# Optimization experiments

Hardware: AMD Instinct MI355X
Metric: run time of the kernel (lower is better)

Reference implementation:

```python
import jax, jax.numpy as jnp
import numpy as np

ALPHA = 0.2          # LeakyReLU negative slope
NEG_INF = -9e15      # mask value used by the torch module


def setup_inputs() -> dict:
    key = jax.random.key(0)
    k1, k2, k3, k4 = jax.random.split(key, 4)
    N, F_IN, F_OUT = 8192, 128, 128
    h = jax.random.normal(k1, (N, F_IN), dtype=jnp.float32)
    adj = jax.random.randint(k2, (N, N), 0, 2, dtype=jnp.int32)
    # xavier_uniform(gain=1.414) approximated with scaled normal init
    W = jax.random.normal(k3, (F_IN, F_OUT), dtype=jnp.float32) * (1.414 / np.sqrt(F_IN))
    a = jax.random.normal(k4, (2 * F_OUT, 1), dtype=jnp.float32) * (1.414 / np.sqrt(2 * F_OUT))
    return {"h": h, "adj": adj, "W": W, "a": a}


def reference(h, adj, W, a):
    # Wh: [N, F]
    Wh = h @ W
    F_out = W.shape[1]
    # e[i,j] = LeakyReLU( [Wh_i || Wh_j] . a ) = LeakyReLU( Wh_i.a1 + Wh_j.a2 )
    e_src = Wh @ a[:F_out, 0]   # [N]
    e_dst = Wh @ a[F_out:, 0]   # [N]
    e = jax.nn.leaky_relu(e_src[:, None] + e_dst[None, :], negative_slope=ALPHA)  # [N, N]
    attention = jax.nn.softmax(jnp.where(adj > 0, e, NEG_INF), axis=1)
    # dropout is identity in eval mode
    h_prime = attention @ Wh    # [N, F]
    return h_prime
```

## Files before the change

kernel.cpp:

```cpp
#include <hip/hip_runtime.h>
#include <hip/hip_bf16.h>


#define NN 8192
#define FF 128
#define SEG 4
#define JSEG (NN / SEG)
#define ITERS (JSEG / 64)

typedef __bf16 bf16x8 __attribute__((ext_vector_type(8)));
typedef float floatx4 __attribute__((ext_vector_type(4)));
typedef int   intx4  __attribute__((ext_vector_type(4)));

__device__ __forceinline__ unsigned short b2u(__bf16 x) {
    return __builtin_bit_cast(unsigned short, x);
}

__global__ __launch_bounds__(512) void k1_wh(const float* __restrict__ h,
                                             const float* __restrict__ W,
                                             const float* __restrict__ a,
                                             unsigned short* __restrict__ WhT,
                                             float* __restrict__ e_src,
                                             float* __restrict__ e_dst) {
    __shared__ float hL[32 * 132];
    __shared__ float wL[128 * 132];
    __shared__ float uL[128], vL[128];
    __shared__ unsigned short tL[128 * 40];

    int t = threadIdx.x;
    int i0 = blockIdx.x * 32;

    {
        int row = t >> 4, c = (t & 15) * 8;
        const float4* s = (const float4*)&h[(i0 + row) * FF + c];
        float4* d = (float4*)&hL[row * 132 + c];
        d[0] = s[0]; d[1] = s[1];
    }
    {
        int row = t >> 2, c = (t & 3) * 32;
        const float4* s = (const float4*)&W[row * FF + c];
        float4* d = (float4*)&wL[row * 132 + c];
        #pragma unroll
        for (int j = 0; j < 8; j++) d[j] = s[j];
    }
    __syncthreads();

    if (t < 256) {
        int k = t & 127;
        const float* ap = a + (t >> 7) * FF;
        float s = 0.f;
        for (int c = 0; c < 128; c += 4) {
            float4 w4 = *(const float4*)&wL[k * 132 + c];
            s = fmaf(w4.x, ap[c], s);     s = fmaf(w4.y, ap[c + 1], s);
            s = fmaf(w4.z, ap[c + 2], s); s = fmaf(w4.w, ap[c + 3], s);
        }
        (t < 128 ? uL : vL)[k] = s * 1.44269504f;
    }

    int r0 = (t & 7) * 4;
    int c0 = (t >> 3) * 2;
    float acc[4][2] = {};
    for (int k0 = 0; k0 < 128; k0 += 4) {
        float4 hr[4]; float2 wr[4];
        #pragma unroll
        for (int i = 0; i < 4; i++) hr[i] = *(const float4*)&hL[(r0 + i) * 132 + k0];
        #pragma unroll
        for (int i = 0; i < 4; i++) wr[i] = *(const float2*)&wL[(k0 + i) * 132 + c0];
        #pragma unroll
        for (int kj = 0; kj < 4; kj++) {
            #pragma unroll
            for (int ri = 0; ri < 4; ri++) {
                float hvv = ((const float*)&hr[ri])[kj];
                acc[ri][0] = fmaf(hvv, wr[kj].x, acc[ri][0]);
                acc[ri][1] = fmaf(hvv, wr[kj].y, acc[ri][1]);
            }
        }
    }
    #pragma unroll
    for (int ri = 0; ri < 4; ri++)
        #pragma unroll
        for (int cj = 0; cj < 2; cj++)
            tL[(c0 + cj) * 40 + r0 + ri] = b2u((__bf16)acc[ri][cj]);
    __syncthreads();

    if (t < 64) {
        int row = t & 31;
        const float* sv = (t < 32) ? uL : vL;
        float s = 0.f;
        for (int k = 0; k < 128; k += 4) {
            float4 h4 = *(const float4*)&hL[row * 132 + k];
            float4 s4 = *(const float4*)&sv[k];
            s = fmaf(h4.x, s4.x, s); s = fmaf(h4.y, s4.y, s);
            s = fmaf(h4.z, s4.z, s); s = fmaf(h4.w, s4.w, s);
        }
        (t < 32 ? e_src : e_dst)[i0 + row] = s;
    }
    {
        int f = t & 127, part = t >> 7;
        const uint4* s = (const uint4*)&tL[f * 40 + part * 8];
        uint4* d = (uint4*)&WhT[f * NN + i0 + part * 8];
        *d = *s;
    }
}

__device__ __forceinline__ float mask_w(int a, float x) {
    float l = fmaxf(x, 0.2f * x);
    float e = __builtin_amdgcn_exp2f(l);
    return a > 0 ? e : 0.f;
}

__device__ __forceinline__ ushort4 pack4(float w0, float w1, float w2, float w3) {
    union { ushort4 u; __bf16 b[4]; } pk;
    pk.b[0] = (__bf16)w0; pk.b[1] = (__bf16)w1;
    pk.b[2] = (__bf16)w2; pk.b[3] = (__bf16)w3;
    return pk.u;
}

__global__ __launch_bounds__(512, 4) void k2_gat(const int* __restrict__ adj,
                                                 const unsigned short* __restrict__ WhT,
                                                 const float* __restrict__ e_src,
                                                 const float* __restrict__ e_dst,
                                                 float* __restrict__ numpart,
                                                 float* __restrict__ denpart) {
    __shared__ unsigned short wt[2][32 * 64];
    __shared__ float esL[32];
    __shared__ float dpart[32 * 17];

    int t = threadIdx.x;
    int bx = blockIdx.x;
    int g = bx >> 2, seg = bx & 3;
    int i0 = g * 32;
    int jbase = seg * JSEG;

    if (t < 32) esL[t] = e_src[i0 + t];

    int q  = t & 15;
    int ii = t >> 4;
    int lane = t & 63, wave = t >> 6;
    int mrow = lane & 15, quad = lane >> 4;
    int n0 = wave * 16;

    const unsigned short* Bb = WhT + (size_t)(n0 + mrow) * NN + jbase + quad * 8;
    const intx4* Ab = (const intx4*)(adj + (size_t)(i0 + ii) * NN + jbase + q * 4);
    const float* Eb = e_dst + jbase + q * 4;

    int waddr = ii * 64 + (((q >> 1) ^ (ii & 7)) << 3) + ((q & 1) << 2);
    int ra00 = mrow * 64 + ((quad ^ (mrow & 7)) << 3);
    int ra01 = mrow * 64 + (((4 + quad) ^ (mrow & 7)) << 3);
    int ra10 = (16 + mrow) * 64 + ((quad ^ (mrow & 7)) << 3);
    int ra11 = (16 + mrow) * 64 + (((4 + quad) ^ (mrow & 7)) << 3);

    floatx4 acc0 = {0.f, 0.f, 0.f, 0.f};
    floatx4 acc1 = {0.f, 0.f, 0.f, 0.f};
    float dsum = 0.f;

    intx4  av0 = __builtin_nontemporal_load(Ab);
    float4 ed0 = *(const float4*)Eb;
    intx4  avB = __builtin_nontemporal_load(Ab + 16);
    float4 edB = *(const float4*)(Eb + 64);
    bf16x8 b0 = *(const bf16x8*)Bb;
    bf16x8 b1 = *(const bf16x8*)(Bb + 32);

    __syncthreads();
    float es_i = esL[ii];

    {
        float w0 = mask_w(av0.x, es_i + ed0.x);
        float w1 = mask_w(av0.y, es_i + ed0.y);
        float w2 = mask_w(av0.z, es_i + ed0.z);
        float w3 = mask_w(av0.w, es_i + ed0.w);
        dsum += (w0 + w1) + (w2 + w3);
        *(ushort4*)&wt[0][waddr] = pack4(w0, w1, w2, w3);
    }
    __syncthreads();

    for (int k = 0; k < ITERS - 1; k++) {
        int jp = ((k + 2 < ITERS) ? (k + 2) : (ITERS - 1));
        intx4  avN = __builtin_nontemporal_load(Ab + jp * 16);
        float4 edN = *(const float4*)(Eb + jp * 64);
        int jn = (k + 1) * 64;
        bf16x8 nb0 = *(const bf16x8*)(Bb + jn);
        bf16x8 nb1 = *(const bf16x8*)(Bb + jn + 32);

        const unsigned short* buf = wt[k & 1];
        bf16x8 a00 = *(const bf16x8*)&buf[ra00];
        bf16x8 a10 = *(const bf16x8*)&buf[ra10];
        bf16x8 a01 = *(const bf16x8*)&buf[ra01];
        bf16x8 a11 = *(const bf16x8*)&buf[ra11];
        acc0 = __builtin_amdgcn_mfma_f32_16x16x32_bf16(a00, b0, acc0, 0, 0, 0);
        acc1 = __builtin_amdgcn_mfma_f32_16x16x32_bf16(a10, b0, acc1, 0, 0, 0);
        acc0 = __builtin_amdgcn_mfma_f32_16x16x32_bf16(a01, b1, acc0, 0, 0, 0);
        acc1 = __builtin_amdgcn_mfma_f32_16x16x32_bf16(a11, b1, acc1, 0, 0, 0);

        float w0 = mask_w(avB.x, es_i + edB.x);
        float w1 = mask_w(avB.y, es_i + edB.y);
        float w2 = mask_w(avB.z, es_i + edB.z);
        float w3 = mask_w(avB.w, es_i + edB.w);
        dsum += (w0 + w1) + (w2 + w3);
        *(ushort4*)&wt[(k + 1) & 1][waddr] = pack4(w0, w1, w2, w3);
        avB = avN; edB = edN;
        b0 = nb0; b1 = nb1;
        __syncthreads();
    }
    {
        const unsigned short* buf = wt[(ITERS - 1) & 1];
        bf16x8 a00 = *(const bf16x8*)&buf[ra00];
        bf16x8 a10 = *(const bf16x8*)&buf[ra10];
        bf16x8 a01 = *(const bf16x8*)&buf[ra01];
        bf16x8 a11 = *(const bf16x8*)&buf[ra11];
        acc0 = __builtin_amdgcn_mfma_f32_16x16x32_bf16(a00, b0, acc0, 0, 0, 0);
        acc1 = __builtin_amdgcn_mfma_f32_16x16x32_bf16(a10, b0, acc1, 0, 0, 0);
        acc0 = __builtin_amdgcn_mfma_f32_16x16x32_bf16(a01, b1, acc0, 0, 0, 0);
        acc1 = __builtin_amdgcn_mfma_f32_16x16x32_bf16(a11, b1, acc1, 0, 0, 0);
    }

    dpart[ii * 17 + q] = dsum;
    __syncthreads();
    if (t < 32) {
        float s = 0.f;
        #pragma unroll
        for (int k = 0; k < 16; k++) s += dpart[t * 17 + k];
        __builtin_nontemporal_store(s, &denpart[seg * NN + i0 + t]);
    }

    float* np = numpart + (size_t)seg * NN * FF;
    #pragma unroll
    for (int r = 0; r < 4; r++) {
        int row0 = quad * 4 + r;
        __builtin_nontemporal_store(acc0[r], &np[(size_t)(i0 + row0) * FF + n0 + mrow]);
        __builtin_nontemporal_store(acc1[r], &np[(size_t)(i0 + 16 + row0) * FF + n0 + mrow]);
    }
}

__global__ __launch_bounds__(256) void k3_merge(const float* __restrict__ np,
                                               const float* __restrict__ dp,
                                               float* __restrict__ out) {
    int idx = blockIdx.x * 256 + threadIdx.x;
    int i = idx >> 5;
    int c = (idx & 31) << 2;
    float d = dp[i] + dp[NN + i] + dp[2 * NN + i] + dp[3 * NN + i];
    float r = 1.0f / d;
    size_t o = (size_t)i * FF + c;
    const size_t S = (size_t)NN * FF;
    float4 a0 = *(const float4*)&np[o];
    float4 a1 = *(const float4*)&np[o + S];
    float4 a2 = *(const float4*)&np[o + 2 * S];
    float4 a3 = *(const float4*)&np[o + 3 * S];
    float4 v;
    v.x = ((a0.x + a1.x) + (a2.x + a3.x)) * r;
    v.y = ((a0.y + a1.y) + (a2.y + a3.y)) * r;
    v.z = ((a0.z + a1.z) + (a2.z + a3.z)) * r;
    v.w = ((a0.w + a1.w) + (a2.w + a3.w)) * r;
    *(float4*)&out[o] = v;
}

extern "C" void kernel_launch(void* const* d_in, const int* in_sizes, int n_in,
                              void* d_out, int out_size, void* d_ws, size_t ws_size,
                              hipStream_t stream) {
    const float* h   = (const float*)d_in[0];
    const int*   adj = (const int*)d_in[1];
    const float* W   = (const float*)d_in[2];
    const float* a   = (const float*)d_in[3];
    float* out = (float*)d_out;

    char* ws = (char*)d_ws;
    unsigned short* WhT = (unsigned short*)ws;
    float* e_src = (float*)(ws + 2097152);
    float* e_dst = e_src + NN;
    float* denpart = e_dst + NN;
    float* numpart = (float*)(ws + (4u << 20));

    k1_wh<<<dim3(256), dim3(512), 0, stream>>>(h, W, a, WhT, e_src, e_dst);
    k2_gat<<<dim3(256 * SEG), dim3(512), 0, stream>>>(adj, WhT, e_src, e_dst, numpart, denpart);
    k3_merge<<<dim3(NN * FF / 4 / 256), dim3(256), 0, stream>>>(numpart, denpart, out);
}
```

Before: 397.8 us.

## Drop split-K segments and fuse normalization into the attention kernel

Removes the 4-way split over the neighbour dimension and the separate merge kernel. Each block now handles 16 rows across the full 8192 columns with 128-wide tiles and writes normalized output directly, with the denominator reduced by wave shuffles. This avoids the numerator and denominator partial buffers and their round trip through global memory. In exchange, each block now owns only 16 rows, so the WhT B-operand is re-read from global memory by twice as many row blocks. The B loads are also no longer prefetched one iteration ahead.

```diff
diff --git a/kernel.cpp b/kernel.cpp
--- a/kernel.cpp
+++ b/kernel.cpp
@@ -4,9 +4,7 @@
 
 #define NN 8192
 #define FF 128
-#define SEG 4
-#define JSEG (NN / SEG)
-#define ITERS (JSEG / 64)
+#define ITERS (NN / 128)
 
 typedef __bf16 bf16x8 __attribute__((ext_vector_type(8)));
 typedef float floatx4 __attribute__((ext_vector_type(4)));
@@ -120,46 +118,39 @@
                                                  const unsigned short* __restrict__ WhT,
                                                  const float* __restrict__ e_src,
                                                  const float* __restrict__ e_dst,
-                                                 float* __restrict__ numpart,
-                                                 float* __restrict__ denpart) {
-    __shared__ unsigned short wt[2][32 * 64];
-    __shared__ float esL[32];
-    __shared__ float dpart[32 * 17];
+                                                 float* __restrict__ out) {
+    __shared__ unsigned short wt[2][16 * 128];
+    __shared__ float esL[16];
+    __shared__ float denL[16];
 
     int t = threadIdx.x;
-    int bx = blockIdx.x;
-    int g = bx >> 2, seg = bx & 3;
-    int i0 = g * 32;
-    int jbase = seg * JSEG;
-
-    if (t < 32) esL[t] = e_src[i0 + t];
-
-    int q  = t & 15;
-    int ii = t >> 4;
+    int i0 = blockIdx.x * 16;
+
+    if (t < 16) esL[t] = e_src[i0 + t];
+
+    int q  = t & 31;
+    int ii = t >> 5;
     int lane = t & 63, wave = t >> 6;
     int mrow = lane & 15, quad = lane >> 4;
     int n0 = wave * 16;
 
-    const unsigned short* Bb = WhT + (size_t)(n0 + mrow) * NN + jbase + quad * 8;
-    const intx4* Ab = (const intx4*)(adj + (size_t)(i0 + ii) * NN + jbase + q * 4);
-    const float* Eb = e_dst + jbase + q * 4;
-
-    int waddr = ii * 64 + (((q >> 1) ^ (ii & 7)) << 3) + ((q & 1) << 2);
-    int ra00 = mrow * 64 + ((quad ^ (mrow & 7)) << 3);
-    int ra01 = mrow * 64 + (((4 + quad) ^ (mrow & 7)) << 3);
-    int ra10 = (16 + mrow) * 64 + ((quad ^ (mrow & 7)) << 3);
-    int ra11 = (16 + mrow) * 64 + (((4 + quad) ^ (mrow & 7)) << 3);
-
-    floatx4 acc0 = {0.f, 0.f, 0.f, 0.f};
-    floatx4 acc1 = {0.f, 0.f, 0.f, 0.f};
+    const unsigned short* Bb = WhT + (size_t)(n0 + mrow) * NN + quad * 8;
+    const intx4* Ab = (const intx4*)(adj + (size_t)(i0 + ii) * NN + q * 4);
+    const float* Eb = e_dst + q * 4;
+
+    int waddr = ii * 128 + (((q >> 1) ^ (ii & 7)) << 3) + ((q & 1) << 2);
+    int ra0 = mrow * 128 + (((0 + quad) ^ (mrow & 7)) << 3);
+    int ra1 = mrow * 128 + (((4 + quad) ^ (mrow & 7)) << 3);
+    int ra2 = mrow * 128 + (((8 + quad) ^ (mrow & 7)) << 3);
+    int ra3 = mrow * 128 + (((12 + quad) ^ (mrow & 7)) << 3);
+
+    floatx4 acc = {0.f, 0.f, 0.f, 0.f};
     float dsum = 0.f;
 
     intx4  av0 = __builtin_nontemporal_load(Ab);
     float4 ed0 = *(const float4*)Eb;
-    intx4  avB = __builtin_nontemporal_load(Ab + 16);
-    float4 edB = *(const float4*)(Eb + 64);
-    bf16x8 b0 = *(const bf16x8*)Bb;
-    bf16x8 b1 = *(const bf16x8*)(Bb + 32);
+    intx4  avB = __builtin_nontemporal_load(Ab + 32);
+    float4 edB = *(const float4*)(Eb + 128);
 
     __syncthreads();
     float es_i = esL[ii];
@@ -176,21 +167,24 @@
 
     for (int k = 0; k < ITERS - 1; k++) {
         int jp = ((k + 2 < ITERS) ? (k + 2) : (ITERS - 1));
-        intx4  avN = __builtin_nontemporal_load(Ab + jp * 16);
-        float4 edN = *(const float4*)(Eb + jp * 64);
-        int jn = (k + 1) * 64;
-        bf16x8 nb0 = *(const bf16x8*)(Bb + jn);
-        bf16x8 nb1 = *(const bf16x8*)(Bb + jn + 32);
+        intx4  avN = __builtin_nontemporal_load(Ab + jp * 32);
+        float4 edN = *(const float4*)(Eb + jp * 128);
+
+        int j0 = k * 128;
+        bf16x8 b0 = *(const bf16x8*)(Bb + j0);
+        bf16x8 b1 = *(const bf16x8*)(Bb + j0 + 32);
+        bf16x8 b2 = *(const bf16x8*)(Bb + j0 + 64);
+        bf16x8 b3 = *(const bf16x8*)(Bb + j0 + 96);
 
         const unsigned short* buf = wt[k & 1];
-        bf16x8 a00 = *(const bf16x8*)&buf[ra00];
-        bf16x8 a10 = *(const bf16x8*)&buf[ra10];
-        bf16x8 a01 = *(const bf16x8*)&buf[ra01];
-        bf16x8 a11 = *(const bf16x8*)&buf[ra11];
-        acc0 = __builtin_amdgcn_mfma_f32_16x16x32_bf16(a00, b0, acc0, 0, 0, 0);
-        acc1 = __builtin_amdgcn_mfma_f32_16x16x32_bf16(a10, b0, acc1, 0, 0, 0);
-        acc0 = __builtin_amdgcn_mfma_f32_16x16x32_bf16(a01, b1, acc0, 0, 0, 0);
-        acc1 = __builtin_amdgcn_mfma_f32_16x16x32_bf16(a11, b1, acc1, 0, 0, 0);
+        bf16x8 a0 = *(const bf16x8*)&buf[ra0];
+        bf16x8 a1 = *(const bf16x8*)&buf[ra1];
+        bf16x8 a2 = *(const bf16x8*)&buf[ra2];
+        bf16x8 a3 = *(const bf16x8*)&buf[ra3];
+        acc = __builtin_amdgcn_mfma_f32_16x16x32_bf16(a0, b0, acc, 0, 0, 0);
+        acc = __builtin_amdgcn_mfma_f32_16x16x32_bf16(a1, b1, acc, 0, 0, 0);
+        acc = __builtin_amdgcn_mfma_f32_16x16x32_bf16(a2, b2, acc, 0, 0, 0);
+        acc = __builtin_amdgcn_mfma_f32_16x16x32_bf16(a3, b3, acc, 0, 0, 0);
 
         float w0 = mask_w(avB.x, es_i + edB.x);
         float w1 = mask_w(avB.y, es_i + edB.y);
@@ -199,59 +193,38 @@
         dsum += (w0 + w1) + (w2 + w3);
         *(ushort4*)&wt[(k + 1) & 1][waddr] = pack4(w0, w1, w2, w3);
         avB = avN; edB = edN;
-        b0 = nb0; b1 = nb1;
         __syncthreads();
     }
     {
+        int j0 = (ITERS - 1) * 128;
+        bf16x8 b0 = *(const bf16x8*)(Bb + j0);
+        bf16x8 b1 = *(const bf16x8*)(Bb + j0 + 32);
+        bf16x8 b2 = *(const bf16x8*)(Bb + j0 + 64);
+        bf16x8 b3 = *(const bf16x8*)(Bb + j0 + 96);
         const unsigned short* buf = wt[(ITERS - 1) & 1];
-        bf16x8 a00 = *(const bf16x8*)&buf[ra00];
-        bf16x8 a10 = *(const bf16x8*)&buf[ra10];
-        bf16x8 a01 = *(const bf16x8*)&buf[ra01];
-        bf16x8 a11 = *(const bf16x8*)&buf[ra11];
-        acc0 = __builtin_amdgcn_mfma_f32_16x16x32_bf16(a00, b0, acc0, 0, 0, 0);
-        acc1 = __builtin_amdgcn_mfma_f32_16x16x32_bf16(a10, b0, acc1, 0, 0, 0);
-        acc0 = __builtin_amdgcn_mfma_f32_16x16x32_bf16(a01, b1, acc0, 0, 0, 0);
-        acc1 = __builtin_amdgcn_mfma_f32_16x16x32_bf16(a11, b1, acc1, 0, 0, 0);
-    }
-
-    dpart[ii * 17 + q] = dsum;
-    __syncthreads();
-    if (t < 32) {
-        float s = 0.f;
-        #pragma unroll
-        for (int k = 0; k < 16; k++) s += dpart[t * 17 + k];
-        __builtin_nontemporal_store(s, &denpart[seg * NN + i0 + t]);
-    }
-
-    float* np = numpart + (size_t)seg * NN * FF;
+        bf16x8 a0 = *(const bf16x8*)&buf[ra0];
+        bf16x8 a1 = *(const bf16x8*)&buf[ra1];
+        bf16x8 a2 = *(const bf16x8*)&buf[ra2];
+        bf16x8 a3 = *(const bf16x8*)&buf[ra3];
+        acc = __builtin_amdgcn_mfma_f32_16x16x32_bf16(a0, b0, acc, 0, 0, 0);
+        acc = __builtin_amdgcn_mfma_f32_16x16x32_bf16(a1, b1, acc, 0, 0, 0);
+        acc = __builtin_amdgcn_mfma_f32_16x16x32_bf16(a2, b2, acc, 0, 0, 0);
+        acc = __builtin_amdgcn_mfma_f32_16x16x32_bf16(a3, b3, acc, 0, 0, 0);
+    }
+
+    dsum += __shfl_xor(dsum, 16);
+    dsum += __shfl_xor(dsum, 8);
+    dsum += __shfl_xor(dsum, 4);
+    dsum += __shfl_xor(dsum, 2);
+    dsum += __shfl_xor(dsum, 1);
+    if (q == 0) denL[ii] = 1.0f / dsum;
+    __syncthreads();
+
     #pragma unroll
     for (int r = 0; r < 4; r++) {
         int row0 = quad * 4 + r;
-        __builtin_nontemporal_store(acc0[r], &np[(size_t)(i0 + row0) * FF + n0 + mrow]);
-        __builtin_nontemporal_store(acc1[r], &np[(size_t)(i0 + 16 + row0) * FF + n0 + mrow]);
-    }
-}
-
-__global__ __launch_bounds__(256) void k3_merge(const float* __restrict__ np,
-                                               const float* __restrict__ dp,
-                                               float* __restrict__ out) {
-    int idx = blockIdx.x * 256 + threadIdx.x;
-    int i = idx >> 5;
-    int c = (idx & 31) << 2;
-    float d = dp[i] + dp[NN + i] + dp[2 * NN + i] + dp[3 * NN + i];
-    float r = 1.0f / d;
-    size_t o = (size_t)i * FF + c;
-    const size_t S = (size_t)NN * FF;
-    float4 a0 = *(const float4*)&np[o];
-    float4 a1 = *(const float4*)&np[o + S];
-    float4 a2 = *(const float4*)&np[o + 2 * S];
-    float4 a3 = *(const float4*)&np[o + 3 * S];
-    float4 v;
-    v.x = ((a0.x + a1.x) + (a2.x + a3.x)) * r;
-    v.y = ((a0.y + a1.y) + (a2.y + a3.y)) * r;
-    v.z = ((a0.z + a1.z) + (a2.z + a3.z)) * r;
-    v.w = ((a0.w + a1.w) + (a2.w + a3.w)) * r;
-    *(float4*)&out[o] = v;
+        out[(size_t)(i0 + row0) * FF + n0 + mrow] = acc[r] * denL[row0];
+    }
 }
 
 extern "C" void kernel_launch(void* const* d_in, const int* in_sizes, int n_in,
@@ -267,10 +240,7 @@
     unsigned short* WhT = (unsigned short*)ws;
     float* e_src = (float*)(ws + 2097152);
     float* e_dst = e_src + NN;
-    float* denpart = e_dst + NN;
-    float* numpart = (float*)(ws + (4u << 20));
 
     k1_wh<<<dim3(256), dim3(512), 0, stream>>>(h, W, a, WhT, e_src, e_dst);
-    k2_gat<<<dim3(256 * SEG), dim3(512), 0, stream>>>(adj, WhT, e_src, e_dst, numpart, denpart);
-    k3_merge<<<dim3(NN * FF / 4 / 256), dim3(256), 0, stream>>>(numpart, denpart, out);
-}
+    k2_gat<<<dim3(NN / 16), dim3(512), 0, stream>>>(adj, WhT, e_src, e_dst, out);
+}
```

New measurement: 443.4 us. +11.5%, slower.
